# Performance work log

Hardware: AMD Instinct MI355X
Metric: run time of the kernel (lower is better)

Reference implementation:

```python
import jax, jax.numpy as jnp
import numpy as np

D = 128          # feature / hidden dim
K = 3            # SortPooling k (hard-coded in Topkpool)
NUM_CLASS = 10
EPS = 1e-5       # BatchNorm eps


def setup_inputs() -> dict:
    key = jax.random.key(0)
    ks = jax.random.split(key, 24)
    G, NPG = 512, 200
    N = G * NPG
    E = 1638400
    inp = {
        "x": jax.random.normal(ks[0], (N, D), jnp.float32),
        "src": jax.random.randint(ks[1], (E,), 0, N),
        "dst": jax.random.randint(ks[2], (E,), 0, N),
        "num_graphs": G,
        "nodes_per_graph": NPG,
    }
    s = 1.0 / np.sqrt(D)
    for i in (1, 2, 3):
        inp[f"W{i}"] = jax.random.uniform(ks[2 + i], (D, D), jnp.float32, -s, s)
        inp[f"b{i}"] = jnp.zeros((D,), jnp.float32)
        inp[f"g{i}"] = jnp.ones((D,), jnp.float32)   # BN gamma
        inp[f"bt{i}"] = jnp.zeros((D,), jnp.float32)  # BN beta
    sp = 1.0 / np.sqrt(K * D)
    for i in range(4):
        inp[f"P{i}w"] = jax.random.uniform(ks[10 + i], (K * D, NUM_CLASS), jnp.float32, -sp, sp)
        inp[f"P{i}b"] = jnp.zeros((NUM_CLASS,), jnp.float32)
    return inp


def _graph_conv(h, src, dst, W, b, n):
    # DGL GraphConv, norm='both': D_in^{-1/2} A (D_out^{-1/2} h) W + b
    one = jnp.ones((src.shape[0],), h.dtype)
    deg_out = jnp.zeros((n,), h.dtype).at[src].add(one)
    deg_in = jnp.zeros((n,), h.dtype).at[dst].add(one)
    h = h * jax.lax.rsqrt(jnp.maximum(deg_out, 1.0))[:, None]
    agg = jax.ops.segment_sum(h[src], dst, num_segments=n)  # [N, D] scatter-add
    agg = agg * jax.lax.rsqrt(jnp.maximum(deg_in, 1.0))[:, None]
    return agg @ W + b


def _bn_relu(h, g, bt):
    mu = h.mean(axis=0)
    var = jnp.mean((h - mu) ** 2, axis=0)  # biased var, torch BN training mode
    return jax.nn.relu((h - mu) * jax.lax.rsqrt(var + EPS) * g + bt)


def _sort_pool(h, G, npg):
    # DGL SortPooling: sort each node's feature vector ascending, then pick
    # top-K nodes per graph by last (max) channel, concatenate features.
    d = h.shape[-1]
    hs = jnp.sort(h, axis=-1).reshape(G, npg, d)
    idx = jax.lax.top_k(hs[:, :, -1], K)[1]                       # [G, K]
    return jnp.take_along_axis(hs, idx[:, :, None], axis=1).reshape(G, K * d)


def reference(x, W1, b1, g1, bt1, W2, b2, g2, bt2, W3, b3, g3, bt3,
              P0w, P0b, P1w, P1b, P2w, P2b, P3w, P3b,
              src, dst, num_graphs, nodes_per_graph):
    n = x.shape[0]
    reps = [x]
    h = x
    for W, b, g, bt in ((W1, b1, g1, bt1), (W2, b2, g2, bt2), (W3, b3, g3, bt3)):
        h = _bn_relu(_graph_conv(h, src, dst, W, b, n), g, bt)
        reps.append(h)
    score = jnp.zeros((num_graphs, NUM_CLASS), x.dtype)
    for h_i, Pw, Pb in zip(reps, (P0w, P1w, P2w, P3w), (P0b, P1b, P2b, P3b)):
        score = score + _sort_pool(h_i, num_graphs, nodes_per_graph) @ Pw + Pb
    return score
```

## Files before the change

### kernel.cpp

```cpp
#include <hip/hip_runtime.h>
#include <hip/hip_bf16.h>

#define D 128
#define KTOP 3
#define NCLS 10
#define EPS 1e-5f
#define GBM 128
#define BCAP 64


__global__ __launch_bounds__(256) void prologue_kernel(
        const int* __restrict__ src,
        int* __restrict__ deg_out, int E,
        const float* __restrict__ x, float* __restrict__ nodemax, int N,
        float* __restrict__ score, const float* __restrict__ pb0,
        const float* __restrict__ pb1, const float* __restrict__ pb2,
        const float* __restrict__ pb3, int G) {
    int b = blockIdx.x;
    int nbDeg = (E + 255) >> 8;
    if (b < nbDeg) {
        int e = b * 256 + threadIdx.x;
        if (e < E) atomicAdd(&deg_out[src[e]], 1);
        return;
    }
    b -= nbDeg;
    int nbR = N >> 3;
    if (b < nbR) {
        int node = b * 8 + (threadIdx.x >> 5);
        int l = threadIdx.x & 31;
        float4 v = *reinterpret_cast<const float4*>(x + (size_t)node * D + 4 * l);
        float m = fmaxf(fmaxf(v.x, v.y), fmaxf(v.z, v.w));
#pragma unroll
        for (int d = 16; d > 0; d >>= 1) m = fmaxf(m, __shfl_xor(m, d, 64));
        if (l == 0) nodemax[node] = m;
        return;
    }
    for (int i = threadIdx.x; i < G * NCLS; i += 256) {
        int c = i % NCLS;
        score[i] = pb0[c] + pb1[c] + pb2[c] + pb3[c];
    }
}

__global__ void csr_scatter(const int* __restrict__ src, const int* __restrict__ dst,
                            const int* __restrict__ deg_out,
                            int* __restrict__ cursor, int2* __restrict__ csrw, int E) {
    int e = blockIdx.x * blockDim.x + threadIdx.x;
    if (e >= E) return;
    int d = dst[e], s = src[e];
    int slot = atomicAdd(&cursor[d], 1);
    if (slot >= BCAP) return;
    int dg = deg_out[s]; if (dg < 1) dg = 1;
    int2 p; p.x = s; p.y = __float_as_int(rsqrtf((float)dg));
    csrw[(size_t)d * BCAP + slot] = p;
}

__global__ void pad_kernel(const int* __restrict__ cursor, int2* __restrict__ csrw, int N) {
    int d = blockIdx.x * blockDim.x + threadIdx.x;
    if (d >= N) return;
    int c = cursor[d]; if (c > BCAP) c = BCAP;
    int end = (c + 7) & ~7;
    int2 z; z.x = 0; z.y = 0;
    for (int i = c; i < end; ++i) csrw[(size_t)d * BCAP + i] = z;
}

__device__ __forceinline__ float4 bnrelu4(float4 v, float4 sc, float4 sh) {
    float4 r;
    r.x = fmaxf(fmaf(v.x, sc.x, sh.x), 0.f);
    r.y = fmaxf(fmaf(v.y, sc.y, sh.y), 0.f);
    r.z = fmaxf(fmaf(v.z, sc.z, sh.z), 0.f);
    r.w = fmaxf(fmaf(v.w, sc.w, sh.w), 0.f);
    return r;
}


__global__ __launch_bounds__(256) void aggregate_head(
        const float* __restrict__ hin, const int* __restrict__ cursor,
        const int2* __restrict__ csrw, float* __restrict__ hout, int nAgg,
        const float* __restrict__ nodemax, const float* __restrict__ Pw,
        float* __restrict__ score, int NPG,
        const float* __restrict__ bns, const float* __restrict__ g,
        const float* __restrict__ bt, float invN) {
    __shared__ float ov[256];
    __shared__ float sv[256];
    __shared__ int   si[256];
    __shared__ int   sel[KTOP];
    __shared__ float sbuf[KTOP][D];
    __shared__ float red[4][NCLS];
    __shared__ float scs[D], shs[D];
    int b = blockIdx.x;
    int t = threadIdx.x;
    bool useBN = (bns != nullptr);
    if (useBN) {
        if (t < D) {
            float mu  = bns[t] * invN;
            float var = bns[D + t] * invN - mu * mu;
            float inv = rsqrtf(var + EPS);
            float s = g[t] * inv;
            scs[t] = s;
            shs[t] = bt[t] - mu * s;
        }
        __syncthreads();
    }
    if (b < nAgg) {
        int node = b * 8 + (t >> 5);
        int l = t & 31;
        int deg = cursor[node];
        int end = (deg + 7) & ~7; if (end > BCAP) end = BCAP;
        const int2* bkt = csrw + (size_t)node * BCAP;
        const float* base = hin + 4 * l;
        float4 sc4, sh4;
        if (useBN) {
            sc4 = *reinterpret_cast<const float4*>(&scs[4 * l]);
            sh4 = *reinterpret_cast<const float4*>(&shs[4 * l]);
        }
        float4 a0 = {0.f, 0.f, 0.f, 0.f}, a1 = a0;
        for (int e = 0; e < end; e += 8) {
            const int4* ce = reinterpret_cast<const int4*>(bkt + e);
            int4 p0 = ce[0], p1 = ce[1], p2 = ce[2], p3 = ce[3];
            float4 v0 = *reinterpret_cast<const float4*>(base + (size_t)p0.x * D);
            float4 v1 = *reinterpret_cast<const float4*>(base + (size_t)p0.z * D);
            float4 v2 = *reinterpret_cast<const float4*>(base + (size_t)p1.x * D);
            float4 v3 = *reinterpret_cast<const float4*>(base + (size_t)p1.z * D);
            float4 v4 = *reinterpret_cast<const float4*>(base + (size_t)p2.x * D);
            float4 v5 = *reinterpret_cast<const float4*>(base + (size_t)p2.z * D);
            float4 v6 = *reinterpret_cast<const float4*>(base + (size_t)p3.x * D);
            float4 v7 = *reinterpret_cast<const float4*>(base + (size_t)p3.z * D);
            if (useBN) {
                v0 = bnrelu4(v0, sc4, sh4); v1 = bnrelu4(v1, sc4, sh4);
                v2 = bnrelu4(v2, sc4, sh4); v3 = bnrelu4(v3, sc4, sh4);
                v4 = bnrelu4(v4, sc4, sh4); v5 = bnrelu4(v5, sc4, sh4);
                v6 = bnrelu4(v6, sc4, sh4); v7 = bnrelu4(v7, sc4, sh4);
            }
            float w0 = __int_as_float(p0.y), w1 = __int_as_float(p0.w);
            float w2 = __int_as_float(p1.y), w3 = __int_as_float(p1.w);
            float w4 = __int_as_float(p2.y), w5 = __int_as_float(p2.w);
            float w6 = __int_as_float(p3.y), w7 = __int_as_float(p3.w);
            a0.x += w0*v0.x; a0.y += w0*v0.y; a0.z += w0*v0.z; a0.w += w0*v0.w;
            a1.x += w1*v1.x; a1.y += w1*v1.y; a1.z += w1*v1.z; a1.w += w1*v1.w;
            a0.x += w2*v2.x; a0.y += w2*v2.y; a0.z += w2*v2.z; a0.w += w2*v2.w;
            a1.x += w3*v3.x; a1.y += w3*v3.y; a1.z += w3*v3.z; a1.w += w3*v3.w;
            a0.x += w4*v4.x; a0.y += w4*v4.y; a0.z += w4*v4.z; a0.w += w4*v4.w;
            a1.x += w5*v5.x; a1.y += w5*v5.y; a1.z += w5*v5.z; a1.w += w5*v5.w;
            a0.x += w6*v6.x; a0.y += w6*v6.y; a0.z += w6*v6.z; a0.w += w6*v6.w;
            a1.x += w7*v7.x; a1.y += w7*v7.y; a1.z += w7*v7.z; a1.w += w7*v7.w;
        }
        float ri = rsqrtf((float)(deg < 1 ? 1 : deg));
        float4 r;
        r.x = (a0.x + a1.x) * ri;
        r.y = (a0.y + a1.y) * ri;
        r.z = (a0.z + a1.z) * ri;
        r.w = (a0.w + a1.w) * ri;
        *reinterpret_cast<float4*>(hout + (size_t)node * D + 4 * l) = r;
        return;
    }

    int gr = b - nAgg;
    ov[t] = (t < NPG) ? nodemax[(size_t)gr * NPG + t] : -3.4e38f;
    __syncthreads();
    for (int ks = 0; ks < KTOP; ++ks) {
        sv[t] = ov[t]; si[t] = t;
        __syncthreads();
        for (int s = 128; s > 0; s >>= 1) {
            if (t < s) {
                float a = sv[t], c = sv[t + s];
                int ia = si[t], ib = si[t + s];
                if (c > a || (c == a && ib < ia)) { sv[t] = c; si[t] = ib; }
            }
            __syncthreads();
        }
        if (t == 0) { sel[ks] = si[0]; ov[si[0]] = -3.4e38f; }
        __syncthreads();
    }
    int u = t >> 7, tl = t & 127;
    {
        float v = hin[((size_t)gr * NPG + sel[u]) * D + tl];
        sbuf[u][tl] = useBN ? fmaxf(fmaf(v, scs[tl], shs[tl]), 0.f) : v;
        if (t < 128) {
            float v2 = hin[((size_t)gr * NPG + sel[2]) * D + t];
            sbuf[2][t] = useBN ? fmaxf(fmaf(v2, scs[t], shs[t]), 0.f) : v2;
        }
    }
    __syncthreads();
    for (int size = 2; size <= D; size <<= 1) {
        for (int stride = size >> 1; stride > 0; stride >>= 1) {
            int ixj = tl ^ stride;
            if (ixj > tl) {
                float a = sbuf[u][tl], c = sbuf[u][ixj];
                bool up = ((tl & size) == 0);
                if ((a > c) == up) { sbuf[u][tl] = c; sbuf[u][ixj] = a; }
            }
            if (t < 128) {
                int ix2 = t ^ stride;
                if (ix2 > t) {
                    float a = sbuf[2][t], c = sbuf[2][ix2];
                    bool up = ((t & size) == 0);
                    if ((a > c) == up) { sbuf[2][t] = c; sbuf[2][ix2] = a; }
                }
            }
            __syncthreads();
        }
    }
    float part[NCLS];
    float v0 = sbuf[u][tl];
    const float* pw0 = Pw + (size_t)(u * D + tl) * NCLS;
#pragma unroll
    for (int c = 0; c < NCLS; ++c) part[c] = v0 * pw0[c];
    if (t < 128) {
        float v2 = sbuf[2][t];
        const float* pw2 = Pw + (size_t)(2 * D + t) * NCLS;
#pragma unroll
        for (int c = 0; c < NCLS; ++c) part[c] += v2 * pw2[c];
    }
    int lane = t & 63, wid = t >> 6;
#pragma unroll
    for (int c = 0; c < NCLS; ++c) {
        float xx = part[c];
#pragma unroll
        for (int o = 32; o > 0; o >>= 1) xx += __shfl_down(xx, o, 64);
        if (lane == 0) red[wid][c] = xx;
    }
    __syncthreads();
    if (t < NCLS)
        atomicAdd(&score[gr * NCLS + t],
                  red[0][t] + red[1][t] + red[2][t] + red[3][t]);
}


__device__ __forceinline__ void gemm_chunk(const float* __restrict__ ain, size_t rowBase,
        int kc, int c0, const float (*Wl)[D], float (&acc)[4][8]) {
#pragma unroll 2
    for (int k4 = 0; k4 < 16; ++k4) {
        const float* ap = ain + rowBase * D + kc + 4 * k4;
        float4 a0 = *reinterpret_cast<const float4*>(ap);
        float4 a1 = *reinterpret_cast<const float4*>(ap + D);
        float4 a2 = *reinterpret_cast<const float4*>(ap + 2 * D);
        float4 a3 = *reinterpret_cast<const float4*>(ap + 3 * D);
#pragma unroll
        for (int j = 0; j < 4; ++j) {
            int kk = 4 * k4 + j;
            float4 w0 = *reinterpret_cast<const float4*>(&Wl[kk][c0]);
            float4 w1 = *reinterpret_cast<const float4*>(&Wl[kk][c0 + 4]);
            float av[4];
            av[0] = (j==0)?a0.x:(j==1)?a0.y:(j==2)?a0.z:a0.w;
            av[1] = (j==0)?a1.x:(j==1)?a1.y:(j==2)?a1.z:a1.w;
            av[2] = (j==0)?a2.x:(j==1)?a2.y:(j==2)?a2.z:a2.w;
            av[3] = (j==0)?a3.x:(j==1)?a3.y:(j==2)?a3.z:a3.w;
            float wv[8] = {w0.x, w0.y, w0.z, w0.w, w1.x, w1.y, w1.z, w1.w};
#pragma unroll
            for (int i = 0; i < 4; ++i)
#pragma unroll
                for (int jj = 0; jj < 8; ++jj) acc[i][jj] += av[i] * wv[jj];
        }
    }
}

__global__ __launch_bounds__(512) void gemm_bn(const float* __restrict__ ain,
        const float* __restrict__ W, const float* __restrict__ bias,
        float* __restrict__ hout, float* __restrict__ bnsums, int N) {
    __shared__ __align__(16) float Wl[64][D];
    int t = threadIdx.x;
    int cg = t & 15;
    int rs = t >> 4;
    int c0 = cg * 8;
    size_t rowBase = (size_t)blockIdx.x * GBM + 4 * rs;

    float acc[4][8];
#pragma unroll
    for (int i = 0; i < 4; ++i)
#pragma unroll
        for (int j = 0; j < 8; ++j) acc[i][j] = 0.f;

    const float4* Wv = reinterpret_cast<const float4*>(W);
    float4* Wd = reinterpret_cast<float4*>(&Wl[0][0]);
    float4 wpre[4];
#pragma unroll
    for (int i = 0; i < 4; ++i) wpre[i] = Wv[t + 512 * i];
#pragma unroll
    for (int i = 0; i < 4; ++i) Wd[t + 512 * i] = wpre[i];
#pragma unroll
    for (int i = 0; i < 4; ++i) wpre[i] = Wv[2048 + t + 512 * i];
    __syncthreads();
    gemm_chunk(ain, rowBase, 0, c0, Wl, acc);
    __syncthreads();
#pragma unroll
    for (int i = 0; i < 4; ++i) Wd[t + 512 * i] = wpre[i];
    __syncthreads();
    gemm_chunk(ain, rowBase, 64, c0, Wl, acc);

    float4 b0 = *reinterpret_cast<const float4*>(&bias[c0]);
    float4 b1 = *reinterpret_cast<const float4*>(&bias[c0 + 4]);
    float bv[8] = {b0.x, b0.y, b0.z, b0.w, b1.x, b1.y, b1.z, b1.w};
    float cs[8], cq[8];
#pragma unroll
    for (int j = 0; j < 8; ++j) { cs[j] = 0.f; cq[j] = 0.f; }
#pragma unroll
    for (int i = 0; i < 4; ++i) {
#pragma unroll
        for (int j = 0; j < 8; ++j) {
            float v = acc[i][j] + bv[j];
            acc[i][j] = v;
            cs[j] += v;
            cq[j] += v * v;
        }
    }
#pragma unroll
    for (int i = 0; i < 4; ++i) {
        size_t row = rowBase + i;
        float4 o0, o1;
        o0.x = acc[i][0]; o0.y = acc[i][1]; o0.z = acc[i][2]; o0.w = acc[i][3];
        o1.x = acc[i][4]; o1.y = acc[i][5]; o1.z = acc[i][6]; o1.w = acc[i][7];
        *reinterpret_cast<float4*>(&hout[row * D + c0])     = o0;
        *reinterpret_cast<float4*>(&hout[row * D + c0 + 4]) = o1;
    }
#pragma unroll
    for (int j = 0; j < 8; ++j) {
        cs[j] += __shfl_xor(cs[j], 16, 64); cq[j] += __shfl_xor(cq[j], 16, 64);
        cs[j] += __shfl_xor(cs[j], 32, 64); cq[j] += __shfl_xor(cq[j], 32, 64);
    }
    __syncthreads();
    float* red = &Wl[0][0];
    int wid = t >> 6, lane = t & 63;
    if (lane < 16) {
#pragma unroll
        for (int j = 0; j < 8; ++j) {
            red[wid * 256 + lane * 16 + j]     = cs[j];
            red[wid * 256 + lane * 16 + 8 + j] = cq[j];
        }
    }
    __syncthreads();
    if (t < 256) {
        float s = 0.f;
#pragma unroll
        for (int w = 0; w < 8; ++w) s += red[w * 256 + t];
        int cgi = t >> 4, r = t & 15;
        int ch = cgi * 8 + (r & 7);
        atomicAdd(&bnsums[(r < 8 ? 0 : D) + ch], s);
    }
}


__global__ __launch_bounds__(256) void bn_nodemax(const float* __restrict__ h,
        const float* __restrict__ bnsums, const float* __restrict__ g,
        const float* __restrict__ bt, float* __restrict__ nodemax, int N, float invN) {
    __shared__ float sc[D], sh[D];
    int t = threadIdx.x;
    if (t < D) {
        float mu  = bnsums[t] * invN;
        float var = bnsums[D + t] * invN - mu * mu;
        float inv = rsqrtf(var + EPS);
        float s = g[t] * inv;
        sc[t] = s;
        sh[t] = bt[t] - mu * s;
    }
    __syncthreads();
    int node = (blockIdx.x * 256 + t) >> 5;
    int l = t & 31;
    if (node >= N) return;
    float4 v = *reinterpret_cast<const float4*>(h + (size_t)node * D + 4 * l);
    float4 a = *reinterpret_cast<const float4*>(&sc[4 * l]);
    float4 b = *reinterpret_cast<const float4*>(&sh[4 * l]);
    v.x = fmaxf(fmaf(v.x, a.x, b.x), 0.f);
    v.y = fmaxf(fmaf(v.y, a.y, b.y), 0.f);
    v.z = fmaxf(fmaf(v.z, a.z, b.z), 0.f);
    v.w = fmaxf(fmaf(v.w, a.w, b.w), 0.f);
    float m = fmaxf(fmaxf(v.x, v.y), fmaxf(v.z, v.w));
#pragma unroll
    for (int d = 16; d > 0; d >>= 1) m = fmaxf(m, __shfl_xor(m, d, 64));
    if (l == 0) nodemax[node] = m;
}


extern "C" void kernel_launch(void* const* d_in, const int* in_sizes, int n_in,
                              void* d_out, int out_size, void* d_ws, size_t ws_size,
                              hipStream_t stream) {
    const float* x   = (const float*)d_in[0];
    const int*   src = (const int*)d_in[1];
    const int*   dst = (const int*)d_in[2];
    const float* W[3]  = {(const float*)d_in[5],  (const float*)d_in[9],  (const float*)d_in[13]};
    const float* bb[3] = {(const float*)d_in[6],  (const float*)d_in[10], (const float*)d_in[14]};
    const float* gg[3] = {(const float*)d_in[7],  (const float*)d_in[11], (const float*)d_in[15]};
    const float* bt[3] = {(const float*)d_in[8],  (const float*)d_in[12], (const float*)d_in[16]};
    const float* Pw[4] = {(const float*)d_in[17], (const float*)d_in[19], (const float*)d_in[21], (const float*)d_in[23]};
    const float* Pb[4] = {(const float*)d_in[18], (const float*)d_in[20], (const float*)d_in[22], (const float*)d_in[24]};

    int N = in_sizes[0] / D;
    int E = in_sizes[1];
    int G = out_size / NCLS;
    int NPG = N / G;
    float* score = (float*)d_out;

    size_t NF = (size_t)N * D;
    float* fws     = (float*)d_ws;
    float* H       = fws;
    float* T       = H + NF;
    float* nodemax = T + NF;
    float* bnsums  = nodemax + N;
    int* deg_out = (int*)(bnsums + 6 * D);
    int* cursor  = deg_out + N;
    int2* csrw   = (int2*)(cursor + N);

    int nbDeg = (E + 255) >> 8;
    int nbR = N >> 3;
    float invN = 1.0f / (float)N;

    hipMemsetAsync(deg_out, 0, sizeof(int) * (size_t)2 * N, stream);
    hipMemsetAsync(bnsums, 0, sizeof(float) * 6 * D, stream);

    prologue_kernel<<<nbDeg + nbR + 1, 256, 0, stream>>>(
        src, deg_out, E, x, nodemax, N,
        score, Pb[0], Pb[1], Pb[2], Pb[3], G);
    csr_scatter<<<(E + 255) / 256, 256, 0, stream>>>(src, dst, deg_out, cursor, csrw, E);
    pad_kernel<<<(N + 255) / 256, 256, 0, stream>>>(cursor, csrw, N);

    int nAgg = N / 8;
    const float* hin = x;
    const float* curBns = nullptr;
    const float* curG = nullptr;
    const float* curBt = nullptr;
    for (int l = 0; l < 3; ++l) {
        float* bns = bnsums + l * 2 * D;
        aggregate_head<<<nAgg + G, 256, 0, stream>>>(
            hin, cursor, csrw, T, nAgg, nodemax, Pw[l], score, NPG,
            curBns, curG, curBt, invN);
        gemm_bn<<<N / GBM, 512, 0, stream>>>(T, W[l], bb[l], H, bns, N);
        bn_nodemax<<<N / 8, 256, 0, stream>>>(H, bns, gg[l], bt[l], nodemax, N, invN);
        hin = H;
        curBns = bns; curG = gg[l]; curBt = bt[l];
    }
    aggregate_head<<<G, 256, 0, stream>>>(
        H, cursor, csrw, T, 0, nodemax, Pw[3], score, NPG,
        curBns, curG, curBt, invN);
}
```

Measured before the change: 833.7 us.

## Store index-only CSR, fold edge scatter into build kernel, prefetch GEMM A-tile

The CSR bucket now stores only source indices (int) instead of (index, weight) pairs, and the per-edge D_out^{-1/2} weight is computed during aggregation from deg_out. Because the scatter no longer needs the finished out-degrees, it is folded into the prologue kernel alongside degree counting, which removes one launch. The GEMM inner loop also register-prefetches the next A float4s ahead of the FMAs. The aim is to halve CSR storage and read traffic and shorten the setup chain. The cost is an extra deg_out gather plus an rsqrt per edge in each of the four aggregation passes.

```diff
diff --git a/kernel.cpp b/kernel.cpp
--- a/kernel.cpp
+++ b/kernel.cpp
@@ -9,9 +9,10 @@
 #define BCAP 64
 
 
-__global__ __launch_bounds__(256) void prologue_kernel(
-        const int* __restrict__ src,
-        int* __restrict__ deg_out, int E,
+__global__ __launch_bounds__(256) void build_kernel(
+        const int* __restrict__ src, const int* __restrict__ dst,
+        int* __restrict__ deg_out, int* __restrict__ cursor,
+        int* __restrict__ csr, int E,
         const float* __restrict__ x, float* __restrict__ nodemax, int N,
         float* __restrict__ score, const float* __restrict__ pb0,
         const float* __restrict__ pb1, const float* __restrict__ pb2,
@@ -24,6 +25,16 @@
         return;
     }
     b -= nbDeg;
+    if (b < nbDeg) {
+        int e = b * 256 + threadIdx.x;
+        if (e < E) {
+            int d = dst[e];
+            int slot = atomicAdd(&cursor[d], 1);
+            if (slot < BCAP) csr[(size_t)d * BCAP + slot] = src[e];
+        }
+        return;
+    }
+    b -= nbDeg;
     int nbR = N >> 3;
     if (b < nbR) {
         int node = b * 8 + (threadIdx.x >> 5);
@@ -41,26 +52,12 @@
     }
 }
 
-__global__ void csr_scatter(const int* __restrict__ src, const int* __restrict__ dst,
-                            const int* __restrict__ deg_out,
-                            int* __restrict__ cursor, int2* __restrict__ csrw, int E) {
-    int e = blockIdx.x * blockDim.x + threadIdx.x;
-    if (e >= E) return;
-    int d = dst[e], s = src[e];
-    int slot = atomicAdd(&cursor[d], 1);
-    if (slot >= BCAP) return;
-    int dg = deg_out[s]; if (dg < 1) dg = 1;
-    int2 p; p.x = s; p.y = __float_as_int(rsqrtf((float)dg));
-    csrw[(size_t)d * BCAP + slot] = p;
-}
-
-__global__ void pad_kernel(const int* __restrict__ cursor, int2* __restrict__ csrw, int N) {
+__global__ void pad_kernel(const int* __restrict__ cursor, int* __restrict__ csr, int N) {
     int d = blockIdx.x * blockDim.x + threadIdx.x;
     if (d >= N) return;
     int c = cursor[d]; if (c > BCAP) c = BCAP;
     int end = (c + 7) & ~7;
-    int2 z; z.x = 0; z.y = 0;
-    for (int i = c; i < end; ++i) csrw[(size_t)d * BCAP + i] = z;
+    for (int i = c; i < end; ++i) csr[(size_t)d * BCAP + i] = 0;
 }
 
 __device__ __forceinline__ float4 bnrelu4(float4 v, float4 sc, float4 sh) {
@@ -72,10 +69,18 @@
     return r;
 }
 
+__device__ __forceinline__ float edgew(int idx, const int* __restrict__ deg_out,
+                                       bool valid) {
+    if (!valid) return 0.f;
+    int dg = deg_out[idx]; if (dg < 1) dg = 1;
+    return rsqrtf((float)dg);
+}
+
 
 __global__ __launch_bounds__(256) void aggregate_head(
         const float* __restrict__ hin, const int* __restrict__ cursor,
-        const int2* __restrict__ csrw, float* __restrict__ hout, int nAgg,
+        const int* __restrict__ csr, const int* __restrict__ deg_out,
+        float* __restrict__ hout, int nAgg,
         const float* __restrict__ nodemax, const float* __restrict__ Pw,
         float* __restrict__ score, int NPG,
         const float* __restrict__ bns, const float* __restrict__ g,
@@ -106,7 +111,7 @@
         int l = t & 31;
         int deg = cursor[node];
         int end = (deg + 7) & ~7; if (end > BCAP) end = BCAP;
-        const int2* bkt = csrw + (size_t)node * BCAP;
+        const int* bkt = csr + (size_t)node * BCAP;
         const float* base = hin + 4 * l;
         float4 sc4, sh4;
         if (useBN) {
@@ -115,26 +120,30 @@
         }
         float4 a0 = {0.f, 0.f, 0.f, 0.f}, a1 = a0;
         for (int e = 0; e < end; e += 8) {
-            const int4* ce = reinterpret_cast<const int4*>(bkt + e);
-            int4 p0 = ce[0], p1 = ce[1], p2 = ce[2], p3 = ce[3];
-            float4 v0 = *reinterpret_cast<const float4*>(base + (size_t)p0.x * D);
-            float4 v1 = *reinterpret_cast<const float4*>(base + (size_t)p0.z * D);
-            float4 v2 = *reinterpret_cast<const float4*>(base + (size_t)p1.x * D);
-            float4 v3 = *reinterpret_cast<const float4*>(base + (size_t)p1.z * D);
-            float4 v4 = *reinterpret_cast<const float4*>(base + (size_t)p2.x * D);
-            float4 v5 = *reinterpret_cast<const float4*>(base + (size_t)p2.z * D);
-            float4 v6 = *reinterpret_cast<const float4*>(base + (size_t)p3.x * D);
-            float4 v7 = *reinterpret_cast<const float4*>(base + (size_t)p3.z * D);
+            int4 i0 = *reinterpret_cast<const int4*>(bkt + e);
+            int4 i1 = *reinterpret_cast<const int4*>(bkt + e + 4);
+            float4 v0 = *reinterpret_cast<const float4*>(base + (size_t)i0.x * D);
+            float4 v1 = *reinterpret_cast<const float4*>(base + (size_t)i0.y * D);
+            float4 v2 = *reinterpret_cast<const float4*>(base + (size_t)i0.z * D);
+            float4 v3 = *reinterpret_cast<const float4*>(base + (size_t)i0.w * D);
+            float4 v4 = *reinterpret_cast<const float4*>(base + (size_t)i1.x * D);
+            float4 v5 = *reinterpret_cast<const float4*>(base + (size_t)i1.y * D);
+            float4 v6 = *reinterpret_cast<const float4*>(base + (size_t)i1.z * D);
+            float4 v7 = *reinterpret_cast<const float4*>(base + (size_t)i1.w * D);
+            float w0 = edgew(i0.x, deg_out, e + 0 < deg);
+            float w1 = edgew(i0.y, deg_out, e + 1 < deg);
+            float w2 = edgew(i0.z, deg_out, e + 2 < deg);
+            float w3 = edgew(i0.w, deg_out, e + 3 < deg);
+            float w4 = edgew(i1.x, deg_out, e + 4 < deg);
+            float w5 = edgew(i1.y, deg_out, e + 5 < deg);
+            float w6 = edgew(i1.z, deg_out, e + 6 < deg);
+            float w7 = edgew(i1.w, deg_out, e + 7 < deg);
             if (useBN) {
                 v0 = bnrelu4(v0, sc4, sh4); v1 = bnrelu4(v1, sc4, sh4);
                 v2 = bnrelu4(v2, sc4, sh4); v3 = bnrelu4(v3, sc4, sh4);
                 v4 = bnrelu4(v4, sc4, sh4); v5 = bnrelu4(v5, sc4, sh4);
                 v6 = bnrelu4(v6, sc4, sh4); v7 = bnrelu4(v7, sc4, sh4);
             }
-            float w0 = __int_as_float(p0.y), w1 = __int_as_float(p0.w);
-            float w2 = __int_as_float(p1.y), w3 = __int_as_float(p1.w);
-            float w4 = __int_as_float(p2.y), w5 = __int_as_float(p2.w);
-            float w6 = __int_as_float(p3.y), w7 = __int_as_float(p3.w);
             a0.x += w0*v0.x; a0.y += w0*v0.y; a0.z += w0*v0.z; a0.w += w0*v0.w;
             a1.x += w1*v1.x; a1.y += w1*v1.y; a1.z += w1*v1.z; a1.w += w1*v1.w;
             a0.x += w2*v2.x; a0.y += w2*v2.y; a0.z += w2*v2.z; a0.w += w2*v2.w;
@@ -228,13 +237,21 @@
 
 __device__ __forceinline__ void gemm_chunk(const float* __restrict__ ain, size_t rowBase,
         int kc, int c0, const float (*Wl)[D], float (&acc)[4][8]) {
+    const float* ap = ain + rowBase * D + kc;
+    float4 a0 = *reinterpret_cast<const float4*>(ap);
+    float4 a1 = *reinterpret_cast<const float4*>(ap + D);
+    float4 a2 = *reinterpret_cast<const float4*>(ap + 2 * D);
+    float4 a3 = *reinterpret_cast<const float4*>(ap + 3 * D);
 #pragma unroll 2
     for (int k4 = 0; k4 < 16; ++k4) {
-        const float* ap = ain + rowBase * D + kc + 4 * k4;
-        float4 a0 = *reinterpret_cast<const float4*>(ap);
-        float4 a1 = *reinterpret_cast<const float4*>(ap + D);
-        float4 a2 = *reinterpret_cast<const float4*>(ap + 2 * D);
-        float4 a3 = *reinterpret_cast<const float4*>(ap + 3 * D);
+        float4 n0 = a0, n1 = a1, n2 = a2, n3 = a3;
+        if (k4 < 15) {
+            const float* np = ap + 4 * (k4 + 1);
+            n0 = *reinterpret_cast<const float4*>(np);
+            n1 = *reinterpret_cast<const float4*>(np + D);
+            n2 = *reinterpret_cast<const float4*>(np + 2 * D);
+            n3 = *reinterpret_cast<const float4*>(np + 3 * D);
+        }
 #pragma unroll
         for (int j = 0; j < 4; ++j) {
             int kk = 4 * k4 + j;
@@ -251,6 +268,7 @@
 #pragma unroll
                 for (int jj = 0; jj < 8; ++jj) acc[i][jj] += av[i] * wv[jj];
         }
+        a0 = n0; a1 = n1; a2 = n2; a3 = n3;
     }
 }
 
@@ -397,7 +415,7 @@
     float* bnsums  = nodemax + N;
     int* deg_out = (int*)(bnsums + 6 * D);
     int* cursor  = deg_out + N;
-    int2* csrw   = (int2*)(cursor + N);
+    int* csr     = cursor + N;
 
     int nbDeg = (E + 255) >> 8;
     int nbR = N >> 3;
@@ -406,11 +424,10 @@
     hipMemsetAsync(deg_out, 0, sizeof(int) * (size_t)2 * N, stream);
     hipMemsetAsync(bnsums, 0, sizeof(float) * 6 * D, stream);
 
-    prologue_kernel<<<nbDeg + nbR + 1, 256, 0, stream>>>(
-        src, deg_out, E, x, nodemax, N,
+    build_kernel<<<2 * nbDeg + nbR + 1, 256, 0, stream>>>(
+        src, dst, deg_out, cursor, csr, E, x, nodemax, N,
         score, Pb[0], Pb[1], Pb[2], Pb[3], G);
-    csr_scatter<<<(E + 255) / 256, 256, 0, stream>>>(src, dst, deg_out, cursor, csrw, E);
-    pad_kernel<<<(N + 255) / 256, 256, 0, stream>>>(cursor, csrw, N);
+    pad_kernel<<<(N + 255) / 256, 256, 0, stream>>>(cursor, csr, N);
 
     int nAgg = N / 8;
     const float* hin = x;
@@ -420,7 +437,7 @@
     for (int l = 0; l < 3; ++l) {
         float* bns = bnsums + l * 2 * D;
         aggregate_head<<<nAgg + G, 256, 0, stream>>>(
-            hin, cursor, csrw, T, nAgg, nodemax, Pw[l], score, NPG,
+            hin, cursor, csr, deg_out, T, nAgg, nodemax, Pw[l], score, NPG,
             curBns, curG, curBt, invN);
         gemm_bn<<<N / GBM, 512, 0, stream>>>(T, W[l], bb[l], H, bns, N);
         bn_nodemax<<<N / 8, 256, 0, stream>>>(H, bns, gg[l], bt[l], nodemax, N, invN);
@@ -428,6 +445,6 @@
         curBns = bns; curG = gg[l]; curBt = bt[l];
     }
     aggregate_head<<<G, 256, 0, stream>>>(
-        H, cursor, csrw, T, 0, nodemax, Pw[3], score, NPG,
+        H, cursor, csr, deg_out, T, 0, nodemax, Pw[3], score, NPG,
         curBns, curG, curBt, invN);
 }
```

Result: slower. 956.8 us (+14.8%).

## Compute per-node max inside head blocks, drop bn_nodemax kernel, prefetch GEMM A tiles

Applied to the files above, without the earlier changes.

Removes the separate bn_nodemax kernel and the nodemax pass in the prologue. Each head block now reads its graph's node rows itself, applies BN+ReLU, and computes the per-node max before top-k selection. This avoids a full extra pass over H per layer plus three kernel launches. The cost is that the head blocks do more serial work, 200 rows read by 8 rows per iteration. Separately, the GEMM inner loop now software-prefetches the next A float4 rows to hide global load latency.

```diff
diff --git a/kernel.cpp b/kernel.cpp
--- a/kernel.cpp
+++ b/kernel.cpp
@@ -12,7 +12,6 @@
 __global__ __launch_bounds__(256) void prologue_kernel(
         const int* __restrict__ src,
         int* __restrict__ deg_out, int E,
-        const float* __restrict__ x, float* __restrict__ nodemax, int N,
         float* __restrict__ score, const float* __restrict__ pb0,
         const float* __restrict__ pb1, const float* __restrict__ pb2,
         const float* __restrict__ pb3, int G) {
@@ -21,18 +20,6 @@
     if (b < nbDeg) {
         int e = b * 256 + threadIdx.x;
         if (e < E) atomicAdd(&deg_out[src[e]], 1);
-        return;
-    }
-    b -= nbDeg;
-    int nbR = N >> 3;
-    if (b < nbR) {
-        int node = b * 8 + (threadIdx.x >> 5);
-        int l = threadIdx.x & 31;
-        float4 v = *reinterpret_cast<const float4*>(x + (size_t)node * D + 4 * l);
-        float m = fmaxf(fmaxf(v.x, v.y), fmaxf(v.z, v.w));
-#pragma unroll
-        for (int d = 16; d > 0; d >>= 1) m = fmaxf(m, __shfl_xor(m, d, 64));
-        if (l == 0) nodemax[node] = m;
         return;
     }
     for (int i = threadIdx.x; i < G * NCLS; i += 256) {
@@ -76,8 +63,7 @@
 __global__ __launch_bounds__(256) void aggregate_head(
         const float* __restrict__ hin, const int* __restrict__ cursor,
         const int2* __restrict__ csrw, float* __restrict__ hout, int nAgg,
-        const float* __restrict__ nodemax, const float* __restrict__ Pw,
-        float* __restrict__ score, int NPG,
+        const float* __restrict__ Pw, float* __restrict__ score, int NPG,
         const float* __restrict__ bns, const float* __restrict__ g,
         const float* __restrict__ bt, float invN) {
     __shared__ float ov[256];
@@ -155,7 +141,29 @@
     }
 
     int gr = b - nAgg;
-    ov[t] = (t < NPG) ? nodemax[(size_t)gr * NPG + t] : -3.4e38f;
+    ov[t] = -3.4e38f;
+    __syncthreads();
+    {
+        int rw = t >> 5;
+        int l  = t & 31;
+        float4 sc4, sh4;
+        if (useBN) {
+            sc4 = *reinterpret_cast<const float4*>(&scs[4 * l]);
+            sh4 = *reinterpret_cast<const float4*>(&shs[4 * l]);
+        }
+        for (int r0 = 0; r0 < NPG; r0 += 8) {
+            int r = r0 + rw;
+            if (r < NPG) {
+                float4 v = *reinterpret_cast<const float4*>(
+                    hin + ((size_t)gr * NPG + r) * D + 4 * l);
+                if (useBN) v = bnrelu4(v, sc4, sh4);
+                float m = fmaxf(fmaxf(v.x, v.y), fmaxf(v.z, v.w));
+#pragma unroll
+                for (int d = 16; d > 0; d >>= 1) m = fmaxf(m, __shfl_xor(m, d, 64));
+                if (l == 0) ov[r] = m;
+            }
+        }
+    }
     __syncthreads();
     for (int ks = 0; ks < KTOP; ++ks) {
         sv[t] = ov[t]; si[t] = t;
@@ -228,13 +236,21 @@
 
 __device__ __forceinline__ void gemm_chunk(const float* __restrict__ ain, size_t rowBase,
         int kc, int c0, const float (*Wl)[D], float (&acc)[4][8]) {
+    const float* ap = ain + rowBase * D + kc;
+    float4 a0 = *reinterpret_cast<const float4*>(ap);
+    float4 a1 = *reinterpret_cast<const float4*>(ap + D);
+    float4 a2 = *reinterpret_cast<const float4*>(ap + 2 * D);
+    float4 a3 = *reinterpret_cast<const float4*>(ap + 3 * D);
 #pragma unroll 2
     for (int k4 = 0; k4 < 16; ++k4) {
-        const float* ap = ain + rowBase * D + kc + 4 * k4;
-        float4 a0 = *reinterpret_cast<const float4*>(ap);
-        float4 a1 = *reinterpret_cast<const float4*>(ap + D);
-        float4 a2 = *reinterpret_cast<const float4*>(ap + 2 * D);
-        float4 a3 = *reinterpret_cast<const float4*>(ap + 3 * D);
+        float4 n0 = a0, n1 = a1, n2 = a2, n3 = a3;
+        if (k4 < 15) {
+            const float* np = ap + 4 * (k4 + 1);
+            n0 = *reinterpret_cast<const float4*>(np);
+            n1 = *reinterpret_cast<const float4*>(np + D);
+            n2 = *reinterpret_cast<const float4*>(np + 2 * D);
+            n3 = *reinterpret_cast<const float4*>(np + 3 * D);
+        }
 #pragma unroll
         for (int j = 0; j < 4; ++j) {
             int kk = 4 * k4 + j;
@@ -251,6 +267,7 @@
 #pragma unroll
                 for (int jj = 0; jj < 8; ++jj) acc[i][jj] += av[i] * wv[jj];
         }
+        a0 = n0; a1 = n1; a2 = n2; a3 = n3;
     }
 }
 
@@ -336,37 +353,6 @@
         int ch = cgi * 8 + (r & 7);
         atomicAdd(&bnsums[(r < 8 ? 0 : D) + ch], s);
     }
-}
-
-
-__global__ __launch_bounds__(256) void bn_nodemax(const float* __restrict__ h,
-        const float* __restrict__ bnsums, const float* __restrict__ g,
-        const float* __restrict__ bt, float* __restrict__ nodemax, int N, float invN) {
-    __shared__ float sc[D], sh[D];
-    int t = threadIdx.x;
-    if (t < D) {
-        float mu  = bnsums[t] * invN;
-        float var = bnsums[D + t] * invN - mu * mu;
-        float inv = rsqrtf(var + EPS);
-        float s = g[t] * inv;
-        sc[t] = s;
-        sh[t] = bt[t] - mu * s;
-    }
-    __syncthreads();
-    int node = (blockIdx.x * 256 + t) >> 5;
-    int l = t & 31;
-    if (node >= N) return;
-    float4 v = *reinterpret_cast<const float4*>(h + (size_t)node * D + 4 * l);
-    float4 a = *reinterpret_cast<const float4*>(&sc[4 * l]);
-    float4 b = *reinterpret_cast<const float4*>(&sh[4 * l]);
-    v.x = fmaxf(fmaf(v.x, a.x, b.x), 0.f);
-    v.y = fmaxf(fmaf(v.y, a.y, b.y), 0.f);
-    v.z = fmaxf(fmaf(v.z, a.z, b.z), 0.f);
-    v.w = fmaxf(fmaf(v.w, a.w, b.w), 0.f);
-    float m = fmaxf(fmaxf(v.x, v.y), fmaxf(v.z, v.w));
-#pragma unroll
-    for (int d = 16; d > 0; d >>= 1) m = fmaxf(m, __shfl_xor(m, d, 64));
-    if (l == 0) nodemax[node] = m;
 }
 
 
@@ -393,22 +379,19 @@
     float* fws     = (float*)d_ws;
     float* H       = fws;
     float* T       = H + NF;
-    float* nodemax = T + NF;
-    float* bnsums  = nodemax + N;
+    float* bnsums  = T + NF;
     int* deg_out = (int*)(bnsums + 6 * D);
     int* cursor  = deg_out + N;
     int2* csrw   = (int2*)(cursor + N);
 
     int nbDeg = (E + 255) >> 8;
-    int nbR = N >> 3;
     float invN = 1.0f / (float)N;
 
     hipMemsetAsync(deg_out, 0, sizeof(int) * (size_t)2 * N, stream);
     hipMemsetAsync(bnsums, 0, sizeof(float) * 6 * D, stream);
 
-    prologue_kernel<<<nbDeg + nbR + 1, 256, 0, stream>>>(
-        src, deg_out, E, x, nodemax, N,
-        score, Pb[0], Pb[1], Pb[2], Pb[3], G);
+    prologue_kernel<<<nbDeg + 1, 256, 0, stream>>>(
+        src, deg_out, E, score, Pb[0], Pb[1], Pb[2], Pb[3], G);
     csr_scatter<<<(E + 255) / 256, 256, 0, stream>>>(src, dst, deg_out, cursor, csrw, E);
     pad_kernel<<<(N + 255) / 256, 256, 0, stream>>>(cursor, csrw, N);
 
@@ -420,14 +403,13 @@
     for (int l = 0; l < 3; ++l) {
         float* bns = bnsums + l * 2 * D;
         aggregate_head<<<nAgg + G, 256, 0, stream>>>(
-            hin, cursor, csrw, T, nAgg, nodemax, Pw[l], score, NPG,
+            hin, cursor, csrw, T, nAgg, Pw[l], score, NPG,
             curBns, curG, curBt, invN);
         gemm_bn<<<N / GBM, 512, 0, stream>>>(T, W[l], bb[l], H, bns, N);
-        bn_nodemax<<<N / 8, 256, 0, stream>>>(H, bns, gg[l], bt[l], nodemax, N, invN);
         hin = H;
         curBns = bns; curG = gg[l]; curBt = bt[l];
     }
     aggregate_head<<<G, 256, 0, stream>>>(
-        H, cursor, csrw, T, 0, nodemax, Pw[3], score, NPG,
+        H, cursor, csrw, T, 0, Pw[3], score, NPG,
         curBns, curG, curBt, invN);
 }
```

Result: no change. 841.2 us (+0.9%).

## Merge CSR scatter into degree pass and fill weights in separate pad pass

Applied to the files above, without the earlier changes.

The dst-bucketed CSR scatter now runs inside the same launch as the out-degree count and writes only source indices. A new per-node pass then reads deg_out to fill in the rsqrt normalisation weights and zero-pad each bucket, replacing the old scatter and pad kernels. Separately, the GEMM inner loop software-prefetches the next A float4 rows so the loads overlap the FMAs. The fused launch drops a kernel boundary at the cost of rereading and rewriting the CSR entries, and the prefetch raises register use.

```diff
diff --git a/kernel.cpp b/kernel.cpp
--- a/kernel.cpp
+++ b/kernel.cpp
@@ -9,9 +9,10 @@
 #define BCAP 64
 
 
-__global__ __launch_bounds__(256) void prologue_kernel(
-        const int* __restrict__ src,
-        int* __restrict__ deg_out, int E,
+__global__ __launch_bounds__(256) void build_kernel(
+        const int* __restrict__ src, const int* __restrict__ dst,
+        int* __restrict__ deg_out, int* __restrict__ cursor,
+        int2* __restrict__ csrw, int E,
         const float* __restrict__ x, float* __restrict__ nodemax, int N,
         float* __restrict__ score, const float* __restrict__ pb0,
         const float* __restrict__ pb1, const float* __restrict__ pb2,
@@ -24,6 +25,17 @@
         return;
     }
     b -= nbDeg;
+    if (b < nbDeg) {
+        int e = b * 256 + threadIdx.x;
+        if (e < E) {
+            int d = dst[e];
+            int slot = atomicAdd(&cursor[d], 1);
+            if (slot < BCAP)
+                reinterpret_cast<int*>(csrw)[((size_t)d * BCAP + slot) * 2] = src[e];
+        }
+        return;
+    }
+    b -= nbDeg;
     int nbR = N >> 3;
     if (b < nbR) {
         int node = b * 8 + (threadIdx.x >> 5);
@@ -41,26 +53,26 @@
     }
 }
 
-__global__ void csr_scatter(const int* __restrict__ src, const int* __restrict__ dst,
-                            const int* __restrict__ deg_out,
-                            int* __restrict__ cursor, int2* __restrict__ csrw, int E) {
-    int e = blockIdx.x * blockDim.x + threadIdx.x;
-    if (e >= E) return;
-    int d = dst[e], s = src[e];
-    int slot = atomicAdd(&cursor[d], 1);
-    if (slot >= BCAP) return;
-    int dg = deg_out[s]; if (dg < 1) dg = 1;
-    int2 p; p.x = s; p.y = __float_as_int(rsqrtf((float)dg));
-    csrw[(size_t)d * BCAP + slot] = p;
-}
-
-__global__ void pad_kernel(const int* __restrict__ cursor, int2* __restrict__ csrw, int N) {
-    int d = blockIdx.x * blockDim.x + threadIdx.x;
-    if (d >= N) return;
-    int c = cursor[d]; if (c > BCAP) c = BCAP;
-    int end = (c + 7) & ~7;
-    int2 z; z.x = 0; z.y = 0;
-    for (int i = c; i < end; ++i) csrw[(size_t)d * BCAP + i] = z;
+
+__global__ __launch_bounds__(256) void wfill_pad(const int* __restrict__ cursor,
+        const int* __restrict__ deg_out, int2* __restrict__ csrw, int N) {
+    int node = blockIdx.x * 4 + (threadIdx.x >> 6);
+    int slot = threadIdx.x & 63;
+    if (node >= N) return;
+    int c = cursor[node]; if (c > BCAP) c = BCAP;
+    int cpad = (c + 7) & ~7;
+    if (slot >= cpad) return;
+    int2* ent = csrw + (size_t)node * BCAP + slot;
+    int2 out;
+    if (slot < c) {
+        int s = ent->x;
+        int dg = deg_out[s]; if (dg < 1) dg = 1;
+        out.x = s;
+        out.y = __float_as_int(rsqrtf((float)dg));
+    } else {
+        out.x = 0; out.y = 0;
+    }
+    *ent = out;
 }
 
 __device__ __forceinline__ float4 bnrelu4(float4 v, float4 sc, float4 sh) {
@@ -228,13 +240,21 @@
 
 __device__ __forceinline__ void gemm_chunk(const float* __restrict__ ain, size_t rowBase,
         int kc, int c0, const float (*Wl)[D], float (&acc)[4][8]) {
+    const float* ap = ain + rowBase * D + kc;
+    float4 a0 = *reinterpret_cast<const float4*>(ap);
+    float4 a1 = *reinterpret_cast<const float4*>(ap + D);
+    float4 a2 = *reinterpret_cast<const float4*>(ap + 2 * D);
+    float4 a3 = *reinterpret_cast<const float4*>(ap + 3 * D);
 #pragma unroll 2
     for (int k4 = 0; k4 < 16; ++k4) {
-        const float* ap = ain + rowBase * D + kc + 4 * k4;
-        float4 a0 = *reinterpret_cast<const float4*>(ap);
-        float4 a1 = *reinterpret_cast<const float4*>(ap + D);
-        float4 a2 = *reinterpret_cast<const float4*>(ap + 2 * D);
-        float4 a3 = *reinterpret_cast<const float4*>(ap + 3 * D);
+        float4 n0 = a0, n1 = a1, n2 = a2, n3 = a3;
+        if (k4 < 15) {
+            const float* np = ap + 4 * (k4 + 1);
+            n0 = *reinterpret_cast<const float4*>(np);
+            n1 = *reinterpret_cast<const float4*>(np + D);
+            n2 = *reinterpret_cast<const float4*>(np + 2 * D);
+            n3 = *reinterpret_cast<const float4*>(np + 3 * D);
+        }
 #pragma unroll
         for (int j = 0; j < 4; ++j) {
             int kk = 4 * k4 + j;
@@ -251,6 +271,7 @@
 #pragma unroll
                 for (int jj = 0; jj < 8; ++jj) acc[i][jj] += av[i] * wv[jj];
         }
+        a0 = n0; a1 = n1; a2 = n2; a3 = n3;
     }
 }
 
@@ -406,11 +427,10 @@
     hipMemsetAsync(deg_out, 0, sizeof(int) * (size_t)2 * N, stream);
     hipMemsetAsync(bnsums, 0, sizeof(float) * 6 * D, stream);
 
-    prologue_kernel<<<nbDeg + nbR + 1, 256, 0, stream>>>(
-        src, deg_out, E, x, nodemax, N,
+    build_kernel<<<2 * nbDeg + nbR + 1, 256, 0, stream>>>(
+        src, dst, deg_out, cursor, csrw, E, x, nodemax, N,
         score, Pb[0], Pb[1], Pb[2], Pb[3], G);
-    csr_scatter<<<(E + 255) / 256, 256, 0, stream>>>(src, dst, deg_out, cursor, csrw, E);
-    pad_kernel<<<(N + 255) / 256, 256, 0, stream>>>(cursor, csrw, N);
+    wfill_pad<<<(N + 3) / 4, 256, 0, stream>>>(cursor, deg_out, csrw, N);
 
     int nAgg = N / 8;
     const float* hin = x;
```

After: 885.1 us. 1.06x slower.
